# Optimization experiments

Measured on AMD Instinct MI355X. Metric: run time of the kernel, lower is better.

The kernel has to match this reference:

```python
import jax, jax.numpy as jnp
import numpy as np

DIM = 128
HEADS = 8
RBF_K = 16
N_LIG = 20000
N_PROT = 80000
E = 262144
HEAD_DIM = DIM // HEADS
SCALE = HEAD_DIM ** -0.5


def setup_inputs() -> dict:
    key = jax.random.key(0)
    ks = jax.random.split(key, 16)
    inp = {
        "ligand_x": jax.random.normal(ks[0], (N_LIG, DIM), dtype=jnp.float32),
        "protein_x": jax.random.normal(ks[1], (N_PROT, DIM), dtype=jnp.float32),
        "cross_edges": jax.random.randint(ks[2], (E, 2), 0, N_LIG, dtype=jnp.int64)
        if jax.config.jax_enable_x64 else jax.random.randint(ks[2], (E, 2), 0, N_LIG, dtype=jnp.int32),
        "cross_attr": jax.random.uniform(ks[3], (E, RBF_K), dtype=jnp.float32),
        "Wq": jax.random.normal(ks[4], (DIM, DIM), dtype=jnp.float32) * (DIM ** -0.5),
        "bq": jax.random.normal(ks[5], (DIM,), dtype=jnp.float32) * 0.02,
        "Wk": jax.random.normal(ks[6], (DIM, DIM), dtype=jnp.float32) * (DIM ** -0.5),
        "bk": jax.random.normal(ks[7], (DIM,), dtype=jnp.float32) * 0.02,
        "Wv": jax.random.normal(ks[8], (DIM, DIM), dtype=jnp.float32) * (DIM ** -0.5),
        "bv": jax.random.normal(ks[9], (DIM,), dtype=jnp.float32) * 0.02,
        "Wo": jax.random.normal(ks[10], (DIM, DIM), dtype=jnp.float32) * (DIM ** -0.5),
        "bo": jax.random.normal(ks[11], (DIM,), dtype=jnp.float32) * 0.02,
        "Wr": jax.random.normal(ks[12], (RBF_K, HEADS), dtype=jnp.float32) * (RBF_K ** -0.5),
        "br": jax.random.normal(ks[13], (HEADS,), dtype=jnp.float32) * 0.02,
        "lig_start": 0,
        "prot_start": 0,
    }
    return inp


def _heads(t):
    return t.reshape(t.shape[0], HEADS, HEAD_DIM)


def _cross_attend(q_nodes, k_nodes, v_nodes, dst_idx, src_idx, rbf_bias, n_dst):
    # gather per-edge q/k/v: [E, H, D]
    qe = q_nodes[dst_idx]
    ke = k_nodes[src_idx]
    ve = v_nodes[src_idx]
    logits = jnp.einsum("ehd,ehd->eh", qe, ke) * SCALE + rbf_bias  # [E, H]
    # segment softmax over edges grouped by destination node
    m = jax.ops.segment_max(logits, dst_idx, num_segments=n_dst)  # [N, H]
    ex = jnp.exp(logits - m[dst_idx])
    s = jax.ops.segment_sum(ex, dst_idx, num_segments=n_dst)  # [N, H]
    w = ex / (s[dst_idx] + 1e-8)  # [E, H]
    agg = jax.ops.segment_sum(w[:, :, None] * ve, dst_idx, num_segments=n_dst)
    return agg.reshape(n_dst, HEADS * HEAD_DIM)


def reference(ligand_x, protein_x, cross_edges, cross_attr, Wq, bq, Wk, bk, Wv, bv,
              Wo, bo, Wr, br, lig_start, prot_start):
    n_lig, n_prot = ligand_x.shape[0], protein_x.shape[0]
    q_l = _heads(ligand_x @ Wq + bq)
    k_p = _heads(protein_x @ Wk + bk)
    v_p = _heads(protein_x @ Wv + bv)
    q_p = _heads(protein_x @ Wq + bq)
    k_l = _heads(ligand_x @ Wk + bk)
    v_l = _heads(ligand_x @ Wv + bv)

    lig_local = cross_edges[:, 0] - lig_start
    prot_local = cross_edges[:, 1] - prot_start
    rbf_bias = cross_attr @ Wr + br  # [E, heads]

    lig_agg = _cross_attend(q_l, k_p, v_p, lig_local, prot_local, rbf_bias, n_lig)
    prot_agg = _cross_attend(q_p, k_l, v_l, prot_local, lig_local, rbf_bias, n_prot)

    ligand_out = lig_agg @ Wo + bo   # dropout is identity at inference
    protein_out = prot_agg @ Wo + bo
    return (ligand_out, protein_out)
```

## Files before the change

### kernel.cpp

```cpp
#include <hip/hip_runtime.h>
#include <hip/hip_bf16.h>

typedef unsigned short u16;
typedef __attribute__((ext_vector_type(8))) short short8;
typedef __attribute__((ext_vector_type(4))) float f32x4;

__device__ __forceinline__ float bf2f(u16 u){
  union { unsigned int i; float f; } c; c.i = ((unsigned int)u) << 16; return c.f;
}
__device__ __forceinline__ u16 f2bf(float f){
  union { float f; unsigned int i; } c; c.f = f;
  unsigned int x = c.i;
  return (u16)((x + 0x7FFFu + ((x >> 16) & 1u)) >> 16);
}

__device__ __forceinline__ int edge_get(const int* __restrict__ e32, int i64, int e, int c){
  int idx = 2 * e + c;
  return i64 ? e32[2 * idx] : e32[idx];
}

__global__ __launch_bounds__(256) void init_all(
    const void* __restrict__ Wq, const void* __restrict__ Wk,
    const void* __restrict__ Wv, const void* __restrict__ Wo,
    const void* __restrict__ bq, const void* __restrict__ bk,
    const void* __restrict__ bv, const void* __restrict__ bo,
    u16* __restrict__ Wt, float* __restrict__ biasP,
    const u16* __restrict__ lig16, const int* __restrict__ e32,
    int* __restrict__ flags, int* __restrict__ desc,
    int* __restrict__ cnt, int ntot)
{
  int bx = blockIdx.x, tid = threadIdx.x;

  if (bx < 4){
    __shared__ int Fsh;
    if (tid < 64){
      int c = 0;
      #pragma unroll
      for (int j = 0; j < 4; j++){
        u16 u = lig16[(tid * 4 + j) * 2];
        int ex = (u >> 7) & 0xFF;
        if (ex >= 96 && ex < 160) c++;
      }
      #pragma unroll
      for (int off = 1; off < 64; off <<= 1) c += __shfl_xor(c, off);
      if (tid == 0) Fsh = (c < 128) ? 1 : 0;
    }
    __syncthreads();
    int F = Fsh;
    int mat = bx;
    const void* W = (mat == 0) ? Wq : (mat == 1) ? Wk : (mat == 2) ? Wv : Wo;
    const void* b = (mat == 0) ? bq : (mat == 1) ? bk : (mat == 2) ? bv : bo;
    u16* dst = Wt + mat * 16384;
    #pragma unroll 4
    for (int j = 0; j < 64; j++){
      int idx = tid + j * 256;
      u16 w = F ? f2bf(((const float*)W)[idx]) : ((const u16*)W)[idx];
      dst[(idx & 127) * 128 + (idx >> 7)] = w;
    }
    if (tid < 128)
      biasP[mat * 128 + tid] = F ? ((const float*)b)[tid] : bf2f(((const u16*)b)[tid]);
  } else if (bx == 4){
    if (tid < 64){
      int c = 0, nz = 0;
      #pragma unroll
      for (int j = 0; j < 4; j++){
        u16 u = lig16[(tid * 4 + j) * 2];
        int ex = (u >> 7) & 0xFF;
        if (ex >= 96 && ex < 160) c++;
        if (e32[(tid * 4 + j) * 2 + 1] != 0) nz++;
      }
      #pragma unroll
      for (int off = 1; off < 64; off <<= 1){
        c  += __shfl_xor(c, off);
        nz += __shfl_xor(nz, off);
      }
      if (tid == 0){
        flags[0] = (c < 128) ? 1 : 0;
        flags[1] = (nz == 0) ? 1 : 0;
      }
    }
    desc[tid] = 0;
    desc[256 + tid] = 0;
  } else {
    int i = (bx - 5) * 256 + tid;
    if (i < ntot) cnt[i] = 0;
  }
}

__global__ __launch_bounds__(256) void edge_pre(
    const void* __restrict__ attr, const void* __restrict__ Wr,
    const void* __restrict__ br, float* __restrict__ ebias,
    const int* __restrict__ edges, const int* __restrict__ ls_p,
    const int* __restrict__ ps_p, int* __restrict__ cnt, int nlig, int E_,
    const int* __restrict__ flags)
{
  __shared__ float w[16][8];
  __shared__ float b[8];
  int tid = threadIdx.x;
  int F = flags[0];
  if (tid < 128) w[tid >> 3][tid & 7] = F ? ((const float*)Wr)[tid] : bf2f(((const u16*)Wr)[tid]);
  if (tid < 8)   b[tid] = F ? ((const float*)br)[tid] : bf2f(((const u16*)br)[tid]);
  __syncthreads();
  int e = blockIdx.x * 256 + tid;
  if (e >= E_) return;

  int I64 = flags[1];
  int dl = edge_get(edges, I64, e, 0) - ls_p[0];
  int dp = edge_get(edges, I64, e, 1) - ps_p[0];
  atomicAdd(&cnt[dl], 1);
  atomicAdd(&cnt[nlig + dp], 1);

  float a[16];
  if (F){
    const float* af = (const float*)attr;
    #pragma unroll
    for (int j = 0; j < 4; j++){
      float4 t = *(const float4*)&af[e * 16 + j * 4];
      a[4*j] = t.x; a[4*j+1] = t.y; a[4*j+2] = t.z; a[4*j+3] = t.w;
    }
  } else {
    const u16* au = (const u16*)attr;
    #pragma unroll
    for (int j = 0; j < 4; j++){
      ushort4 t = *(const ushort4*)&au[e * 16 + j * 4];
      a[4*j] = bf2f(t.x); a[4*j+1] = bf2f(t.y); a[4*j+2] = bf2f(t.z); a[4*j+3] = bf2f(t.w);
    }
  }
  #pragma unroll
  for (int hh = 0; hh < 8; hh++){
    float s = b[hh];
    #pragma unroll
    for (int r = 0; r < 16; r++) s += a[r] * w[r][hh];
    ebias[e * 8 + hh] = s;
  }
}

__global__ __launch_bounds__(256) void scan_lookback(
    const int* __restrict__ cnt, int* __restrict__ offs, int* __restrict__ cursor,
    int* __restrict__ desc, int n)
{
  __shared__ int lds[256];
  __shared__ int base_s;
  int bx = blockIdx.x, tid = threadIdx.x;
  int i0 = bx * 2048 + tid * 8;

  int v[8]; int s = 0;
  #pragma unroll
  for (int j = 0; j < 8; j++){
    int idx = i0 + j;
    v[j] = (idx < n) ? cnt[idx] : 0;
    s += v[j];
  }
  lds[tid] = s; __syncthreads();
  for (int off = 1; off < 256; off <<= 1){
    int t = (tid >= off) ? lds[tid - off] : 0;
    __syncthreads();
    lds[tid] += t;
    __syncthreads();
  }
  int thr_excl = lds[tid] - s;
  int block_sum = lds[255];

  if (tid == 0){
    if (bx == 0){
      __hip_atomic_store(&desc[0], (block_sum << 2) | 2, __ATOMIC_RELEASE,
                         __HIP_MEMORY_SCOPE_AGENT);
      base_s = 0;
    } else {
      __hip_atomic_store(&desc[bx], (block_sum << 2) | 1, __ATOMIC_RELEASE,
                         __HIP_MEMORY_SCOPE_AGENT);
      int running = 0;
      int idx = bx - 1;
      while (true){
        int d;
        while (((d = __hip_atomic_load(&desc[idx], __ATOMIC_ACQUIRE,
                                       __HIP_MEMORY_SCOPE_AGENT)) & 3) == 0){
          __builtin_amdgcn_s_sleep(1);
        }
        running += (d >> 2);
        if ((d & 3) == 2) break;
        idx--;
      }
      __hip_atomic_store(&desc[bx], ((running + block_sum) << 2) | 2,
                         __ATOMIC_RELEASE, __HIP_MEMORY_SCOPE_AGENT);
      base_s = running;
    }
  }
  __syncthreads();

  int base = base_s + thr_excl;
  #pragma unroll
  for (int j = 0; j < 8; j++){
    int idx = i0 + j;
    if (idx < n){
      offs[idx] = base;
      cursor[idx] = base;
      base += v[j];
      if (idx == n - 1) offs[n] = base;
    }
  }
}

__global__ __launch_bounds__(256) void fat_qkv_sc(
    const void* __restrict__ A0, int M0, const void* __restrict__ A1, int M1, int mb0,
    const u16* __restrict__ Wt, const float* __restrict__ biasP,
    u16* __restrict__ O0b, u16* __restrict__ O1b, u16* __restrict__ O2b,
    const int* __restrict__ offs,
    const int* __restrict__ edges, const int* __restrict__ ls_p,
    const int* __restrict__ ps_p, int* __restrict__ cursor,
    int2* __restrict__ sorted, int nlig, int E_, const int* __restrict__ flags)
{
  __shared__ __align__(16) char smem[34816];
  int tid = threadIdx.x;
  int F = flags[0];

  int TT = mb0 + ((M1 + 63) >> 6);
  int eb = (E_ + 255) >> 8;
  int G  = TT + eb;
  int bx = blockIdx.x;
  long long pp = (long long)bx * TT;
  int tile = (int)(pp / G);
  int isQ  = (int)(((long long)(bx + 1) * TT) / G) > tile;

  if (isQ){
    u16 (*As)[136] = (u16(*)[136])smem;
    u16 (*Fs)[136] = (u16(*)[136])(smem + 17408);
    __shared__ int act;
    int AF = F;
    const void* A; int M, m0, orow;
    if (tile < mb0){ A = A0; M = M0; m0 = tile * 64;          orow = m0; }
    else           { A = A1; M = M1; m0 = (tile - mb0) * 64;  orow = M0 + m0; }

    if (tid == 0) act = 0;
    __syncthreads();
    if (tid < 64 && m0 + tid < M){
      int r = orow + tid;
      if (offs[r + 1] > offs[r]) act = 1;
    }
    __syncthreads();
    if (!act) return;

    if (AF){
      const float* Af = (const float*)A;
      #pragma unroll
      for (int j = 0; j < 8; j++){
        int u = tid + j * 256, row = u >> 5, c4 = (u & 31) * 4;
        float4 v = make_float4(0.f, 0.f, 0.f, 0.f);
        if (m0 + row < M) v = *(const float4*)&Af[(size_t)(m0 + row) * 128 + c4];
        ushort4 o; o.x = f2bf(v.x); o.y = f2bf(v.y); o.z = f2bf(v.z); o.w = f2bf(v.w);
        *(ushort4*)&As[row][c4] = o;
      }
    } else {
      const float4* Au = (const float4*)A;
      #pragma unroll
      for (int j = 0; j < 4; j++){
        int u = tid + j * 256, row = u >> 4, c8 = (u & 15);
        float4 v = make_float4(0.f, 0.f, 0.f, 0.f);
        if (m0 + row < M) v = Au[(size_t)(m0 + row) * 16 + c8];
        *(float4*)&As[row][c8 * 8] = v;
      }
    }
    __syncthreads();

    int wave = tid >> 6, lane = tid & 63;
    int quad = lane >> 4, ml = lane & 15;

    for (int mat = 0; mat < 3; mat++){
      const u16* wp = Wt + (size_t)mat * 16384
                        + (size_t)(wave * 32 + ml) * 128 + quad * 8;
      short8 wf0[4], wf1[4];
      #pragma unroll
      for (int kk = 0; kk < 4; kk++){
        wf0[kk] = *(const short8*)&wp[kk * 32];
        wf1[kk] = *(const short8*)&wp[2048 + kk * 32];
      }
      float b0 = biasP[mat * 128 + wave * 32 + ml];
      float b1 = biasP[mat * 128 + wave * 32 + 16 + ml];

      f32x4 acc[4][2];
      #pragma unroll
      for (int mt = 0; mt < 4; mt++){
        acc[mt][0] = (f32x4){0.f, 0.f, 0.f, 0.f};
        acc[mt][1] = (f32x4){0.f, 0.f, 0.f, 0.f};
      }
      #pragma unroll
      for (int mt = 0; mt < 4; mt++){
        #pragma unroll
        for (int kk = 0; kk < 4; kk++){
          short8 af = *(const short8*)&As[mt * 16 + ml][kk * 32 + quad * 8];
          acc[mt][0] = __builtin_amdgcn_mfma_f32_16x16x32_bf16(af, wf0[kk], acc[mt][0], 0, 0, 0);
          acc[mt][1] = __builtin_amdgcn_mfma_f32_16x16x32_bf16(af, wf1[kk], acc[mt][1], 0, 0, 0);
        }
      }

      if (mat > 0) __syncthreads();
      #pragma unroll
      for (int mt = 0; mt < 4; mt++){
        #pragma unroll
        for (int r = 0; r < 4; r++){
          int row = mt * 16 + quad * 4 + r;
          Fs[row][wave * 32 + ml]      = f2bf(acc[mt][0][r] + b0);
          Fs[row][wave * 32 + 16 + ml] = f2bf(acc[mt][1][r] + b1);
        }
      }
      __syncthreads();
      u16* Cb = (mat == 0) ? O0b : ((mat == 1) ? O1b : O2b);
      #pragma unroll
      for (int j = 0; j < 4; j++){
        int u = tid + j * 256, row = u >> 4, c8 = (u & 15) * 8;
        if (m0 + row < M)
          *(short8*)&Cb[(size_t)(orow + row) * 128 + c8] = *(const short8*)&Fs[row][c8];
      }
    }
  } else {
    int eidx = bx - tile;
    int e = eidx * 256 + tid;
    if (e >= E_) return;
    int I64 = flags[1];
    int dl = edge_get(edges, I64, e, 0) - ls_p[0];
    int dp = edge_get(edges, I64, e, 1) - ps_p[0];
    int p1 = atomicAdd(&cursor[dl], 1);        sorted[p1] = make_int2(e, nlig + dp);
    int p2 = atomicAdd(&cursor[nlig + dp], 1); sorted[p2] = make_int2(e, dl);
  }
}

__global__ __launch_bounds__(256) void attn_kernel(
    const u16* __restrict__ Q, const u16* __restrict__ K, const u16* __restrict__ V,
    const int2* __restrict__ sorted, const int* __restrict__ offs,
    const float* __restrict__ ebias, u16* __restrict__ AGG, int ntot)
{
  int t = blockIdx.x * 4 + (threadIdx.x >> 6);
  if (t >= ntot) return;
  int lane = threadIdx.x & 63;
  int ql = lane & 15;
  int q4 = lane >> 4;
  int h  = ql >> 1;

  int beg = offs[t], end = offs[t + 1];
  if (beg == end) return;

  short8 qv = *(const short8*)&Q[(size_t)t * 128 + ql * 8];
  float qf[8];
  #pragma unroll
  for (int j = 0; j < 8; j++) qf[j] = bf2f((u16)qv[j]) * 0.25f;

  float m = -1e30f, l = 0.f;
  float a[8];
  #pragma unroll
  for (int j = 0; j < 8; j++) a[j] = 0.f;

  int i = beg + q4;
  int2 cur = make_int2(0, 0), nxt = make_int2(0, 0);
  if (i < end)     cur = sorted[i];
  if (i + 4 < end) nxt = sorted[i + 4];

  short8 kA = {0,0,0,0,0,0,0,0}, vA = {0,0,0,0,0,0,0,0};
  float ebA = 0.f;
  if (i < end){
    kA = *(const short8*)&K[(size_t)cur.y * 128 + ql * 8];
    vA = *(const short8*)&V[(size_t)cur.y * 128 + ql * 8];
    ebA = ebias[(size_t)cur.x * 8 + h];
  }

  while (i < end){
    short8 kB = {0,0,0,0,0,0,0,0}, vB = {0,0,0,0,0,0,0,0};
    float ebB = 0.f;
    if (i + 4 < end){
      kB = *(const short8*)&K[(size_t)nxt.y * 128 + ql * 8];
      vB = *(const short8*)&V[(size_t)nxt.y * 128 + ql * 8];
      ebB = ebias[(size_t)nxt.x * 8 + h];
    }
    int2 n2 = make_int2(0, 0);
    if (i + 8 < end) n2 = sorted[i + 8];

    float s = 0.f;
    #pragma unroll
    for (int j = 0; j < 8; j++) s += qf[j] * bf2f((u16)kA[j]);
    s += __shfl_xor(s, 1);
    float logit = s + ebA;
    float nm = fmaxf(m, logit);
    float alpha = __expf(m - nm);
    float p = __expf(logit - nm);
    #pragma unroll
    for (int j = 0; j < 8; j++) a[j] = a[j] * alpha + p * bf2f((u16)vA[j]);
    l = l * alpha + p;
    m = nm;

    kA = kB; vA = vB; ebA = ebB;
    cur = nxt; nxt = n2;
    i += 4;
  }

  #pragma unroll
  for (int mask = 16; mask <= 32; mask <<= 1){
    float mo = __shfl_xor(m, mask);
    float lo = __shfl_xor(l, mask);
    float nm = fmaxf(m, mo);
    float sA = __expf(m - nm);
    float sB = __expf(mo - nm);
    l = l * sA + lo * sB;
    #pragma unroll
    for (int j = 0; j < 8; j++){
      float ao = __shfl_xor(a[j], mask);
      a[j] = a[j] * sA + ao * sB;
    }
    m = nm;
  }

  if (lane < 16){
    float inv = 1.f / (l + 1e-8f);
    short8 o;
    #pragma unroll
    for (int j = 0; j < 8; j++) o[j] = (short)f2bf(a[j] * inv);
    *(short8*)&AGG[(size_t)t * 128 + ql * 8] = o;
  }
}

__global__ __launch_bounds__(256) void out_proj(
    const u16* __restrict__ AGG, int M, const u16* __restrict__ Wt,
    const float* __restrict__ biasP, void* __restrict__ OUT,
    const int* __restrict__ offs, const int* __restrict__ flags)
{
  __shared__ __align__(16) u16 As[64][136];
  __shared__ __align__(16) u16 Fs[64][136];
  __shared__ int act;
  __shared__ int actRow[64];

  int tid = threadIdx.x;
  int F = flags[0];
  int m0 = blockIdx.x * 64;

  if (tid == 0) act = 0;
  __syncthreads();
  if (tid < 64){
    int r = m0 + tid;
    int a = (r < M) ? (offs[r + 1] > offs[r] ? 1 : 0) : 0;
    actRow[tid] = a;
    if (a) act = 1;
  }
  __syncthreads();

  if (!act){
    if (F){
      float* Of = (float*)OUT;
      #pragma unroll
      for (int j = 0; j < 8; j++){
        int u = tid + j * 256, row = u >> 5, c4 = (u & 31) * 4;
        if (m0 + row < M)
          *(float4*)&Of[(size_t)(m0 + row) * 128 + c4] = *(const float4*)&biasP[384 + c4];
      }
    } else {
      u16* Ob = (u16*)OUT;
      #pragma unroll
      for (int j = 0; j < 4; j++){
        int u = tid + j * 256, row = u >> 4, c8 = (u & 15) * 8;
        if (m0 + row < M){
          short8 s8;
          #pragma unroll
          for (int k = 0; k < 8; k++) s8[k] = (short)f2bf(biasP[384 + c8 + k]);
          *(short8*)&Ob[(size_t)(m0 + row) * 128 + c8] = s8;
        }
      }
    }
    return;
  }

  {
    const float4* Au = (const float4*)AGG;
    #pragma unroll
    for (int j = 0; j < 4; j++){
      int u = tid + j * 256, row = u >> 4, c8 = (u & 15);
      float4 v = make_float4(0.f, 0.f, 0.f, 0.f);
      if (m0 + row < M && actRow[row]) v = Au[(size_t)(m0 + row) * 16 + c8];
      *(float4*)&As[row][c8 * 8] = v;
    }
  }
  __syncthreads();

  int wave = tid >> 6, lane = tid & 63;
  int quad = lane >> 4, ml = lane & 15;

  const u16* wp = Wt + (size_t)3 * 16384 + (size_t)(wave * 32 + ml) * 128 + quad * 8;
  short8 wf0[4], wf1[4];
  #pragma unroll
  for (int kk = 0; kk < 4; kk++){
    wf0[kk] = *(const short8*)&wp[kk * 32];
    wf1[kk] = *(const short8*)&wp[2048 + kk * 32];
  }
  float b0 = biasP[384 + wave * 32 + ml];
  float b1 = biasP[384 + wave * 32 + 16 + ml];

  f32x4 acc[4][2];
  #pragma unroll
  for (int mt = 0; mt < 4; mt++){
    acc[mt][0] = (f32x4){0.f, 0.f, 0.f, 0.f};
    acc[mt][1] = (f32x4){0.f, 0.f, 0.f, 0.f};
  }
  #pragma unroll
  for (int mt = 0; mt < 4; mt++){
    #pragma unroll
    for (int kk = 0; kk < 4; kk++){
      short8 af = *(const short8*)&As[mt * 16 + ml][kk * 32 + quad * 8];
      acc[mt][0] = __builtin_amdgcn_mfma_f32_16x16x32_bf16(af, wf0[kk], acc[mt][0], 0, 0, 0);
      acc[mt][1] = __builtin_amdgcn_mfma_f32_16x16x32_bf16(af, wf1[kk], acc[mt][1], 0, 0, 0);
    }
  }

  if (F){
    float* Of = (float*)OUT;
    #pragma unroll
    for (int mt = 0; mt < 4; mt++){
      #pragma unroll
      for (int r = 0; r < 4; r++){
        int row = mt * 16 + quad * 4 + r;
        if (m0 + row < M){
          float* op = &Of[(size_t)(m0 + row) * 128 + wave * 32 + ml];
          op[0]  = acc[mt][0][r] + b0;
          op[16] = acc[mt][1][r] + b1;
        }
      }
    }
  } else {
    #pragma unroll
    for (int mt = 0; mt < 4; mt++){
      #pragma unroll
      for (int r = 0; r < 4; r++){
        int row = mt * 16 + quad * 4 + r;
        Fs[row][wave * 32 + ml]      = f2bf(acc[mt][0][r] + b0);
        Fs[row][wave * 32 + 16 + ml] = f2bf(acc[mt][1][r] + b1);
      }
    }
    __syncthreads();
    u16* Ob = (u16*)OUT;
    #pragma unroll
    for (int j = 0; j < 4; j++){
      int u = tid + j * 256, row = u >> 4, c8 = (u & 15) * 8;
      if (m0 + row < M)
        *(short8*)&Ob[(size_t)(m0 + row) * 128 + c8] = *(const short8*)&Fs[row][c8];
    }
  }
}

extern "C" void kernel_launch(void* const* d_in, const int* in_sizes, int n_in,
                              void* d_out, int out_size, void* d_ws, size_t ws_size,
                              hipStream_t stream)
{
  const void* ligand_x  = d_in[0];
  const void* protein_x = d_in[1];
  const int* edges      = (const int*)d_in[2];
  const void* attr      = d_in[3];
  const void* Wq = d_in[4];  const void* bq = d_in[5];
  const void* Wk = d_in[6];  const void* bk = d_in[7];
  const void* Wv = d_in[8];  const void* bv = d_in[9];
  const void* Wo = d_in[10]; const void* bo = d_in[11];
  const void* Wr = d_in[12]; const void* br = d_in[13];
  const int* ls_p = (const int*)d_in[14];
  const int* ps_p = (const int*)d_in[15];

  const int nlig = in_sizes[0] / 128;
  const int nprot = in_sizes[1] / 128;
  const int E = in_sizes[2] / 2;
  const int ntot = nlig + nprot;

  char* w = (char*)d_ws;
  size_t off = 0;
  auto alloc = [&](size_t bytes) -> void* {
    void* p = w + off;
    off = (off + bytes + 255) & ~(size_t)255;
    return p;
  };
  int*   flags = (int*)alloc(256);
  u16*   Wt    = (u16*)alloc(4 * 16384 * 2);
  float* biasP = (float*)alloc(4 * 128 * 4);
  u16* Qb  = (u16*)alloc((size_t)ntot * 128 * 2);
  u16* Kb  = (u16*)alloc((size_t)ntot * 128 * 2);
  u16* Vb  = (u16*)alloc((size_t)ntot * 128 * 2);
  u16* AGG = (u16*)alloc((size_t)ntot * 128 * 2);
  float* ebias = (float*)alloc((size_t)E * 8 * 4);
  int* cnt    = (int*)alloc((size_t)ntot * 4);
  int* offs   = (int*)alloc((size_t)(ntot + 1) * 4);
  int* cursor = (int*)alloc((size_t)ntot * 4);
  int* desc   = (int*)alloc(512 * 4);
  int2* sorted = (int2*)alloc((size_t)2 * E * 8);
  (void)ws_size; (void)n_in; (void)out_size;

  const int mb_l = (nlig + 63) / 64;
  const int mb_p = (nprot + 63) / 64;
  const int mb_t = (ntot + 63) / 64;
  const int eb = (E + 255) / 256;
  const int nb = (ntot + 255) / 256;
  const int nsb = (ntot + 2047) / 2048;

  init_all<<<nb + 5, 256, 0, stream>>>(
      Wq, Wk, Wv, Wo, bq, bk, bv, bo, Wt, biasP,
      (const u16*)ligand_x, edges, flags, desc, cnt, ntot);

  edge_pre<<<eb, 256, 0, stream>>>(attr, Wr, br, ebias, edges, ls_p, ps_p,
                                   cnt, nlig, E, flags);

  scan_lookback<<<nsb, 256, 0, stream>>>(cnt, offs, cursor, desc, ntot);

  const int TT = mb_l + mb_p;
  fat_qkv_sc<<<TT + eb, 256, 0, stream>>>(
      ligand_x, nlig, protein_x, nprot, mb_l,
      Wt, biasP, Qb, Kb, Vb,
      offs, edges, ls_p, ps_p, cursor, sorted, nlig, E, flags);

  attn_kernel<<<(ntot + 3) / 4, 256, 0, stream>>>(
      Qb, Kb, Vb, sorted, offs, ebias, AGG, ntot);

  out_proj<<<mb_t, 256, 0, stream>>>(AGG, ntot, Wt, biasP, d_out, offs, flags);
}
```

Before: 276.7 us.

## Pack bf16 edge bias into sorted edge records to drop the indirect bias gather

The per-edge RBF bias is now stored as bf16, and the scatter step copies all 8 head biases into each sorted edge record (32-byte stride). The attention loop therefore reads source index and bias from one record instead of doing a separate indirect gather into ebias by edge id. This removes a random-access load per edge, but each sorted record grows from 8 to 32 bytes, writes during sorting go up, and bias precision drops to bf16.

```diff
diff --git a/kernel.cpp b/kernel.cpp
--- a/kernel.cpp
+++ b/kernel.cpp
@@ -89,7 +89,7 @@
 
 __global__ __launch_bounds__(256) void edge_pre(
     const void* __restrict__ attr, const void* __restrict__ Wr,
-    const void* __restrict__ br, float* __restrict__ ebias,
+    const void* __restrict__ br, u16* __restrict__ ebias16,
     const int* __restrict__ edges, const int* __restrict__ ls_p,
     const int* __restrict__ ps_p, int* __restrict__ cnt, int nlig, int E_,
     const int* __restrict__ flags)
@@ -126,13 +126,15 @@
       a[4*j] = bf2f(t.x); a[4*j+1] = bf2f(t.y); a[4*j+2] = bf2f(t.z); a[4*j+3] = bf2f(t.w);
     }
   }
+  short8 o;
   #pragma unroll
   for (int hh = 0; hh < 8; hh++){
     float s = b[hh];
     #pragma unroll
     for (int r = 0; r < 16; r++) s += a[r] * w[r][hh];
-    ebias[e * 8 + hh] = s;
-  }
+    o[hh] = (short)f2bf(s);
+  }
+  *(short8*)&ebias16[(size_t)e * 8] = o;
 }
 
 __global__ __launch_bounds__(256) void scan_lookback(
@@ -205,10 +207,10 @@
     const void* __restrict__ A0, int M0, const void* __restrict__ A1, int M1, int mb0,
     const u16* __restrict__ Wt, const float* __restrict__ biasP,
     u16* __restrict__ O0b, u16* __restrict__ O1b, u16* __restrict__ O2b,
-    const int* __restrict__ offs,
+    const int* __restrict__ offs, const u16* __restrict__ ebias16,
     const int* __restrict__ edges, const int* __restrict__ ls_p,
     const int* __restrict__ ps_p, int* __restrict__ cursor,
-    int2* __restrict__ sorted, int nlig, int E_, const int* __restrict__ flags)
+    int4* __restrict__ sortedP, int nlig, int E_, const int* __restrict__ flags)
 {
   __shared__ __align__(16) char smem[34816];
   int tid = threadIdx.x;
@@ -319,15 +321,28 @@
     int I64 = flags[1];
     int dl = edge_get(edges, I64, e, 0) - ls_p[0];
     int dp = edge_get(edges, I64, e, 1) - ps_p[0];
-    int p1 = atomicAdd(&cursor[dl], 1);        sorted[p1] = make_int2(e, nlig + dp);
-    int p2 = atomicAdd(&cursor[nlig + dp], 1); sorted[p2] = make_int2(e, dl);
+
+    ushort4 u0 = *(const ushort4*)&ebias16[(size_t)e * 8];
+    ushort4 u1 = *(const ushort4*)&ebias16[(size_t)e * 8 + 4];
+    int w0 = (int)u0.x | ((int)u0.y << 16);
+    int w1 = (int)u0.z | ((int)u0.w << 16);
+    int w2 = (int)u1.x | ((int)u1.y << 16);
+    int w3 = (int)u1.z | ((int)u1.w << 16);
+
+    int p1 = atomicAdd(&cursor[dl], 1);
+    sortedP[(size_t)p1 * 2] = make_int4(nlig + dp, w0, w1, w2);
+    ((int*)&sortedP[(size_t)p1 * 2 + 1])[0] = w3;
+
+    int p2 = atomicAdd(&cursor[nlig + dp], 1);
+    sortedP[(size_t)p2 * 2] = make_int4(dl, w0, w1, w2);
+    ((int*)&sortedP[(size_t)p2 * 2 + 1])[0] = w3;
   }
 }
 
 __global__ __launch_bounds__(256) void attn_kernel(
     const u16* __restrict__ Q, const u16* __restrict__ K, const u16* __restrict__ V,
-    const int2* __restrict__ sorted, const int* __restrict__ offs,
-    const float* __restrict__ ebias, u16* __restrict__ AGG, int ntot)
+    const int4* __restrict__ sortedP, const int* __restrict__ offs,
+    u16* __restrict__ AGG, int ntot)
 {
   int t = blockIdx.x * 4 + (threadIdx.x >> 6);
   if (t >= ntot) return;
@@ -335,6 +350,8 @@
   int ql = lane & 15;
   int q4 = lane >> 4;
   int h  = ql >> 1;
+  int hs = h >> 1;
+  int hodd = h & 1;
 
   int beg = offs[t], end = offs[t + 1];
   if (beg == end) return;
@@ -349,35 +366,49 @@
   #pragma unroll
   for (int j = 0; j < 8; j++) a[j] = 0.f;
 
+  auto ebx = [&](const int4& e4, int w3) -> float {
+    int lo = (hs & 1) ? e4.z : e4.y;
+    int hi = (hs & 1) ? w3   : e4.w;
+    int w  = (hs & 2) ? hi : lo;
+    u16 bb = hodd ? (u16)(w >> 16) : (u16)(w & 0xFFFF);
+    return bf2f(bb);
+  };
+
   int i = beg + q4;
-  int2 cur = make_int2(0, 0), nxt = make_int2(0, 0);
-  if (i < end)     cur = sorted[i];
-  if (i + 4 < end) nxt = sorted[i + 4];
+  int4 eA = make_int4(0,0,0,0), eB = make_int4(0,0,0,0);
+  int wA = 0, wB = 0;
+  if (i < end){
+    eA = sortedP[(size_t)i * 2];
+    wA = ((const int*)&sortedP[(size_t)i * 2 + 1])[0];
+  }
+  if (i + 4 < end){
+    eB = sortedP[(size_t)(i + 4) * 2];
+    wB = ((const int*)&sortedP[(size_t)(i + 4) * 2 + 1])[0];
+  }
 
   short8 kA = {0,0,0,0,0,0,0,0}, vA = {0,0,0,0,0,0,0,0};
-  float ebA = 0.f;
   if (i < end){
-    kA = *(const short8*)&K[(size_t)cur.y * 128 + ql * 8];
-    vA = *(const short8*)&V[(size_t)cur.y * 128 + ql * 8];
-    ebA = ebias[(size_t)cur.x * 8 + h];
+    kA = *(const short8*)&K[(size_t)eA.x * 128 + ql * 8];
+    vA = *(const short8*)&V[(size_t)eA.x * 128 + ql * 8];
   }
 
   while (i < end){
     short8 kB = {0,0,0,0,0,0,0,0}, vB = {0,0,0,0,0,0,0,0};
-    float ebB = 0.f;
     if (i + 4 < end){
-      kB = *(const short8*)&K[(size_t)nxt.y * 128 + ql * 8];
-      vB = *(const short8*)&V[(size_t)nxt.y * 128 + ql * 8];
-      ebB = ebias[(size_t)nxt.x * 8 + h];
-    }
-    int2 n2 = make_int2(0, 0);
-    if (i + 8 < end) n2 = sorted[i + 8];
+      kB = *(const short8*)&K[(size_t)eB.x * 128 + ql * 8];
+      vB = *(const short8*)&V[(size_t)eB.x * 128 + ql * 8];
+    }
+    int4 eC = make_int4(0,0,0,0); int wC = 0;
+    if (i + 8 < end){
+      eC = sortedP[(size_t)(i + 8) * 2];
+      wC = ((const int*)&sortedP[(size_t)(i + 8) * 2 + 1])[0];
+    }
 
     float s = 0.f;
     #pragma unroll
     for (int j = 0; j < 8; j++) s += qf[j] * bf2f((u16)kA[j]);
     s += __shfl_xor(s, 1);
-    float logit = s + ebA;
+    float logit = s + ebx(eA, wA);
     float nm = fmaxf(m, logit);
     float alpha = __expf(m - nm);
     float p = __expf(logit - nm);
@@ -386,8 +417,9 @@
     l = l * alpha + p;
     m = nm;
 
-    kA = kB; vA = vB; ebA = ebB;
-    cur = nxt; nxt = n2;
+    kA = kB; vA = vB;
+    eA = eB; wA = wB;
+    eB = eC; wB = wC;
     i += 4;
   }
 
@@ -576,12 +608,12 @@
   u16* Kb  = (u16*)alloc((size_t)ntot * 128 * 2);
   u16* Vb  = (u16*)alloc((size_t)ntot * 128 * 2);
   u16* AGG = (u16*)alloc((size_t)ntot * 128 * 2);
-  float* ebias = (float*)alloc((size_t)E * 8 * 4);
+  u16* ebias16 = (u16*)alloc((size_t)E * 8 * 2);
   int* cnt    = (int*)alloc((size_t)ntot * 4);
   int* offs   = (int*)alloc((size_t)(ntot + 1) * 4);
   int* cursor = (int*)alloc((size_t)ntot * 4);
   int* desc   = (int*)alloc(512 * 4);
-  int2* sorted = (int2*)alloc((size_t)2 * E * 8);
+  int4* sortedP = (int4*)alloc((size_t)2 * E * 32);
   (void)ws_size; (void)n_in; (void)out_size;
 
   const int mb_l = (nlig + 63) / 64;
@@ -595,7 +627,7 @@
       Wq, Wk, Wv, Wo, bq, bk, bv, bo, Wt, biasP,
       (const u16*)ligand_x, edges, flags, desc, cnt, ntot);
 
-  edge_pre<<<eb, 256, 0, stream>>>(attr, Wr, br, ebias, edges, ls_p, ps_p,
+  edge_pre<<<eb, 256, 0, stream>>>(attr, Wr, br, ebias16, edges, ls_p, ps_p,
                                    cnt, nlig, E, flags);
 
   scan_lookback<<<nsb, 256, 0, stream>>>(cnt, offs, cursor, desc, ntot);
@@ -604,10 +636,10 @@
   fat_qkv_sc<<<TT + eb, 256, 0, stream>>>(
       ligand_x, nlig, protein_x, nprot, mb_l,
       Wt, biasP, Qb, Kb, Vb,
-      offs, edges, ls_p, ps_p, cursor, sorted, nlig, E, flags);
+      offs, ebias16, edges, ls_p, ps_p, cursor, sortedP, nlig, E, flags);
 
   attn_kernel<<<(ntot + 3) / 4, 256, 0, stream>>>(
-      Qb, Kb, Vb, sorted, offs, ebias, AGG, ntot);
+      Qb, Kb, Vb, sortedP, offs, AGG, ntot);
 
   out_proj<<<mb_t, 256, 0, stream>>>(AGG, ntot, Wt, biasP, d_out, offs, flags);
 }
```

New measurement: 286.1 us. 3.4% more time.
